# Optimization experiments

Measured on AMD Instinct MI355X. Metric: run time of the kernel, lower is better.

Reference implementation:

```python
import jax, jax.numpy as jnp
import numpy as np

EPS = 1e-5

def _bilinear_sample(xb, ys, xs):
    # xb: [C,H,W]; ys, xs: [H,W] float sample coordinates (zero outside bounds)
    C, H, W = xb.shape
    y0 = jnp.floor(ys); x0 = jnp.floor(xs)
    y1 = y0 + 1.0;      x1 = x0 + 1.0
    wy1 = ys - y0; wy0 = 1.0 - wy1
    wx1 = xs - x0; wx0 = 1.0 - wx1
    def g(yi, xi):
        valid = (yi >= 0) & (yi < H) & (xi >= 0) & (xi < W)
        yc = jnp.clip(yi, 0, H - 1).astype(jnp.int32)
        xc = jnp.clip(xi, 0, W - 1).astype(jnp.int32)
        return xb[:, yc, xc] * valid[None].astype(xb.dtype)  # [C,H,W]
    return (g(y0, x0) * (wy0 * wx0)[None] + g(y0, x1) * (wy0 * wx1)[None]
          + g(y1, x0) * (wy1 * wx0)[None] + g(y1, x1) * (wy1 * wx1)[None])

def _deform_conv2d(x, offset, mask, w, b):
    # x:[B,C,H,W] offset:[B,18,H,W] mask:[B,9,H,W] w:[Co,C,3,3] b:[Co]
    B, C, H, W = x.shape
    Co = w.shape[0]
    ii = jnp.arange(H, dtype=x.dtype)[:, None]
    jj = jnp.arange(W, dtype=x.dtype)[None, :]
    cols = []
    for k in range(9):  # fixed 3x3 kernel positions, row-major (dy=offset[2k], dx=offset[2k+1])
        ky, kx = k // 3 - 1, k % 3 - 1
        ys = ii + ky + offset[:, 2 * k]      # [B,H,W]
        xs = jj + kx + offset[:, 2 * k + 1]
        v = jax.vmap(_bilinear_sample)(x, ys, xs)  # [B,C,H,W]
        cols.append(v * mask[:, k][:, None])
    cols = jnp.stack(cols, axis=1)               # [B,9,C,H,W]
    out = jnp.einsum('bkchw,ock->bohw', cols, w.reshape(Co, C, 9))
    return out + b[None, :, None, None]

def setup_inputs() -> dict:
    key = jax.random.key(0)
    k1, k2, k3, k4 = jax.random.split(key, 4)
    B, Cin, Cout, H, W = 8, 64, 64, 128, 128
    x = jax.random.normal(k1, (B, Cin, H, W), dtype=jnp.float32)
    # offset/mask conv: small weights so learned offsets stay O(1) pixels;
    # bias[18:]=2.0 as in the module's init (masks start near sigmoid(2))
    w_off = jax.random.normal(k2, (27, Cin, 3, 3), dtype=jnp.float32) * 0.01
    b_off = jnp.concatenate([jnp.zeros((18,), jnp.float32), jnp.full((9,), 2.0, jnp.float32)])
    w_dcn = jax.random.normal(k3, (Cout, Cin, 3, 3), dtype=jnp.float32) / np.sqrt(Cin * 9)
    b_dcn = jax.random.normal(k4, (Cout,), dtype=jnp.float32) * 0.01
    return {"x": x, "w_off": w_off, "b_off": b_off, "w_dcn": w_dcn, "b_dcn": b_dcn}

def reference(x, w_off, b_off, w_dcn, b_dcn):
    dn = ('NCHW', 'OIHW', 'NCHW')
    om = jax.lax.conv_general_dilated(x, w_off, (1, 1), 'SAME', dimension_numbers=dn)
    om = om + b_off[None, :, None, None]
    offset = om[:, :18]
    mask = jax.nn.sigmoid(om[:, 18:])
    y = _deform_conv2d(x, offset, mask, w_dcn, b_dcn)
    # InstanceNorm2d (affine=False, biased variance) + ReLU
    mu = jnp.mean(y, axis=(2, 3), keepdims=True)
    var = jnp.var(y, axis=(2, 3), keepdims=True)
    y = (y - mu) * jax.lax.rsqrt(var + EPS)
    return jax.nn.relu(y)
```

## Files before the change

kernel.cpp:

```cpp
#include <hip/hip_runtime.h>
#include <hip/hip_fp16.h>

#define BB   8
#define CIN  64
#define COUT 64
#define HH   128
#define WW   128
#define HWSZ (HH * WW)

typedef _Float16 f16x8 __attribute__((ext_vector_type(8)));
typedef _Float16 h2v   __attribute__((ext_vector_type(2)));
typedef float    f32x4 __attribute__((ext_vector_type(4)));

__device__ __forceinline__ unsigned short f2h_u(float f) {
    __half h = __float2half(f);
    return __half_as_ushort(h);
}
__device__ __forceinline__ float h2f_u(unsigned short u) {
    _Float16 f = *(_Float16*)&u;
    return (float)f;
}
__device__ __forceinline__ unsigned duph(float f) {
    unsigned u = (unsigned)f2h_u(f);
    return u | (u << 16);
}
__device__ __forceinline__ unsigned pk2h(float lo, float hi) {
    return (unsigned)f2h_u(lo) | ((unsigned)f2h_u(hi) << 16);
}
__device__ __forceinline__ h2v dupL(unsigned u) { h2v v = *(h2v*)&u; return (h2v){v[0], v[0]}; }
__device__ __forceinline__ h2v dupH(unsigned u) { h2v v = *(h2v*)&u; return (h2v){v[1], v[1]}; }

__device__ __forceinline__ unsigned comb2h(unsigned a, unsigned b, unsigned c, unsigned d,
                                           h2v W0, h2v W1, h2v W2, h2v W3) {
    h2v A = *(h2v*)&a, B = *(h2v*)&b, C = *(h2v*)&c, D = *(h2v*)&d;
    h2v r = A * W0;
    r += B * W1;
    r += C * W2;
    r += D * W3;
    return *(unsigned*)&r;
}


__global__ __launch_bounds__(256) void k_tr(const float* __restrict__ x,
                                            const float* __restrict__ wd,
                                            const float* __restrict__ wof,
                                            unsigned short* __restrict__ xT,
                                            unsigned short* __restrict__ wdT,
                                            unsigned short* __restrict__ wofT,
                                            float4* __restrict__ sums4)
{
    const int t = threadIdx.x;
    const int id = blockIdx.x;
    if (id >= 512) {
        if (id == 512) sums4[t] = make_float4(0.f, 0.f, 0.f, 0.f);
        int base = (id - 512) * 256 + t;
#pragma unroll
        for (int j = 0; j < 4; ++j) {
            int idx = base + j * 16384;
            if (idx < 36864) {
                int k = idx >> 12, rem = idx & 4095, co = rem >> 6, c = rem & 63;
                wdT[idx] = f2h_u(wd[(co * 64 + c) * 9 + k]);
            } else if (idx < 55296) {
                int jj = idx - 36864;
                int k = jj >> 11, rem = jj & 2047, o = rem >> 6, c = rem & 63;
                wofT[jj] = (o < 27) ? f2h_u(wof[(o * 64 + c) * 9 + k]) : 0;
            }
        }
        return;
    }
    __shared__ unsigned short tile[256 * 66];
    const int b = id & 7;
    const int p0 = (id >> 3) * 256;
#pragma unroll
    for (int i = 0; i < 16; ++i) {
        int c = i * 4 + (t >> 6);
        int pl = (t & 63) * 4;
        float4 v = *(const float4*)(x + (((size_t)b * 64 + c) << 14) + p0 + pl);
        tile[(pl + 0) * 66 + c] = f2h_u(v.x);
        tile[(pl + 1) * 66 + c] = f2h_u(v.y);
        tile[(pl + 2) * 66 + c] = f2h_u(v.z);
        tile[(pl + 3) * 66 + c] = f2h_u(v.w);
    }
    __syncthreads();
#pragma unroll
    for (int i = 0; i < 8; ++i) {
        int idd = i * 256 + t;
        int pt = idd >> 3, ck = idd & 7;
        const unsigned* srcp = (const unsigned*)&tile[pt * 66 + ck * 8];
        uint4 r;
        r.x = srcp[0]; r.y = srcp[1]; r.z = srcp[2]; r.w = srcp[3];
        *(uint4*)(xT + ((size_t)b << 20) + ((size_t)(ck >> 2) << 19)
                     + (size_t)(p0 + pt) * 32 + (ck & 3) * 8) = r;
    }
}

__global__ __launch_bounds__(256, 2) void k_off(
    const unsigned short* __restrict__ xT, const unsigned short* __restrict__ wofT,
    const float* __restrict__ bof, unsigned short* __restrict__ om)
{
    __shared__ unsigned short tile[8 * 521 * 8];
    const int t = threadIdx.x;
    const int lane = t & 63, wv = t >> 6;
    const int q = lane >> 4, l15 = lane & 15;
    const int b = blockIdx.x & 7;
    const int xblk = blockIdx.x >> 3;
    const int h0 = xblk * 2;
    const int r0 = h0 - 1;
    const unsigned short* xb = xT + ((size_t)b << 20);

#pragma unroll
    for (int i = 0; i < 17; ++i) {
        int id = i * 256 + t;
        if (id < 4160) {
            int m = id & 7, lin = id >> 3;
            int row = lin / 130, col = lin % 130;
            int gy = r0 + row, gx = col - 1;
            uint4 v = {0u, 0u, 0u, 0u};
            if (((unsigned)gy < (unsigned)HH) && ((unsigned)gx < (unsigned)WW))
                v = *(const uint4*)(xb + ((size_t)(m >> 2) << 19)
                                       + (size_t)(gy * WW + gx) * 32 + (m & 3) * 8);
            *(uint4*)&tile[(m * 521 + lin) * 8] = v;
        }
    }
    __syncthreads();

    const int hrow = h0 + (wv >> 1);
    const int c0 = (wv & 1) * 64;

    f32x4 acc[2][4];
#pragma unroll
    for (int mt = 0; mt < 2; ++mt)
#pragma unroll
        for (int nt = 0; nt < 4; ++nt) acc[mt][nt] = (f32x4){0.f, 0.f, 0.f, 0.f};

#pragma unroll
    for (int k = 0; k < 9; ++k) {
        const int ky = k / 3 - 1, kx = k % 3 - 1;
        const int trow = (hrow - h0) + ky + 1;
        const unsigned short* wk = wofT + k * 2048;
#pragma unroll
        for (int ks = 0; ks < 2; ++ks) {
            f16x8 af[2], bfr[4];
#pragma unroll
            for (int mt = 0; mt < 2; ++mt)
                af[mt] = *(const f16x8*)(wk + (mt * 16 + l15) * 64 + ks * 32 + q * 8);
#pragma unroll
            for (int nt = 0; nt < 4; ++nt) {
                int tc = c0 + nt * 16 + l15 + kx + 1;
                bfr[nt] = *(const f16x8*)&tile[((ks * 4 + q) * 521 + trow * 130 + tc) * 8];
            }
#pragma unroll
            for (int mt = 0; mt < 2; ++mt)
#pragma unroll
                for (int nt = 0; nt < 4; ++nt)
                    acc[mt][nt] = __builtin_amdgcn_mfma_f32_16x16x32_f16(
                        af[mt], bfr[nt], acc[mt][nt], 0, 0, 0);
        }
    }

    const int p0 = xblk * 256 + wv * 64;
    unsigned short* omb = om + (size_t)b * 27 * HWSZ;
#pragma unroll
    for (int mt = 0; mt < 2; ++mt)
#pragma unroll
        for (int r = 0; r < 4; ++r) {
            int o = mt * 16 + q * 4 + r;
            if (o < 27) {
                float bias = bof[o];
#pragma unroll
                for (int nt = 0; nt < 4; ++nt) {
                    int pp = p0 + nt * 16 + l15;
                    float v = acc[mt][nt][r] + bias;
                    if (o >= 18) v = 1.f / (1.f + __expf(-v));
                    omb[(size_t)o * HWSZ + pp] = f2h_u(v);
                }
            }
        }
}

__global__ __launch_bounds__(256, 2) void k_dcn(
    const unsigned short* __restrict__ xT, const unsigned short* __restrict__ om,
    const unsigned short* __restrict__ wdT, const float* __restrict__ bd,
    float* __restrict__ out, float2* __restrict__ sums)
{
    __shared__ unsigned short tile_sh[6 * 128 * 32];
    __shared__ uint4          meta_sh[4][64];
    __shared__ float          redS[4][64];
    __shared__ float          redQ[4][64];

    const int t = threadIdx.x;
    const int lane = t & 63, wv = t >> 6;
    const int q = lane >> 4, l15 = lane & 15;
    const int b = blockIdx.x & 7;
    const int pblk = (blockIdx.x >> 3) * 256;
    const int p = pblk + t;
    const int h = p >> 7, w = p & 127;
    const int h0 = pblk >> 7;
    const unsigned short* xbS = xT + ((size_t)b << 20);
    const unsigned short* omp = om + (size_t)b * 27 * HWSZ + p;
    const int gch = q * 8;

    f32x4 acc[4][4];
#pragma unroll
    for (int mt = 0; mt < 4; ++mt)
#pragma unroll
        for (int g = 0; g < 4; ++g) acc[mt][g] = (f32x4){0.f, 0.f, 0.f, 0.f};

#define LOADG2(P, g) { \
    unsigned d0_ = M[g].x; \
    unsigned b0_ = (d0_ & 0x000fffffu) + gch; \
    unsigned sx_ = (d0_ >> 19) & 32u;       \
    unsigned sy_ = (d0_ >> 13) & 4096u;     \
    unsigned b1_ = b0_ + sx_; \
    if (__builtin_expect((int)(d0_ >> 31), 0)) { \
        P[0] = *(const uint4*)(xbh + b0_); \
        P[1] = *(const uint4*)(xbh + b1_); \
        P[2] = *(const uint4*)(xbh + b0_ + sy_); \
        P[3] = *(const uint4*)(xbh + b1_ + sy_); \
    } else { \
        P[0] = *(const uint4*)&tile_sh[b0_]; \
        P[1] = *(const uint4*)&tile_sh[b1_]; \
        P[2] = *(const uint4*)&tile_sh[b0_ + sy_]; \
        P[3] = *(const uint4*)&tile_sh[b1_ + sy_]; \
    } }

#define COMB2(DST, P, g) { \
    h2v W0_ = dupL(M[g].y), W2_ = dupH(M[g].y); \
    h2v W1_ = dupL(M[g].z), W3_ = dupH(M[g].z); \
    uint4 R_; \
    R_.x = comb2h(P[0].x, P[1].x, P[2].x, P[3].x, W0_, W1_, W2_, W3_); \
    R_.y = comb2h(P[0].y, P[1].y, P[2].y, P[3].y, W0_, W1_, W2_, W3_); \
    R_.z = comb2h(P[0].z, P[1].z, P[2].z, P[3].z, W0_, W1_, W2_, W3_); \
    R_.w = comb2h(P[0].w, P[1].w, P[2].w, P[3].w, W0_, W1_, W2_, W3_); \
    DST = *(f16x8*)&R_; }

    for (int hf = 0; hf < 2; ++hf) {
        __syncthreads();
        const unsigned short* xbh = xbS + (hf << 19);
#pragma unroll
        for (int i = 0; i < 12; ++i) {
            int idx = i * 256 + t;
            int s = idx >> 9, u = idx & 511;
            int y = h0 - 2 + s;
            y = min(max(y, 0), HH - 1);
            uint4 v = *(const uint4*)(xbh + (size_t)y * (WW * 32) + u * 8);
            *(uint4*)&tile_sh[idx * 8] = v;
        }
        __syncthreads();

        float offy = h2f_u(omp[0]);
        float offx = h2f_u(omp[HWSZ]);
        float mk   = h2f_u(omp[18 * HWSZ]);

        for (int k = 0; k < 9; ++k) {
            float ys = (float)(h + (k / 3) - 1) + offy;
            float xs = (float)(w + (k % 3) - 1) + offx;
            float fy0 = floorf(ys), fx0 = floorf(xs);
            float wy1 = ys - fy0, wx1 = xs - fx0;
            float wy0 = 1.f - wy1, wx0 = 1.f - wx1;
            int y0 = (int)fy0, x0 = (int)fx0;
            int y1 = y0 + 1, x1 = x0 + 1;
            bool vy0 = (y0 >= 0) && (y0 < HH), vy1 = (y1 >= 0) && (y1 < HH);
            bool vx0 = (x0 >= 0) && (x0 < WW), vx1 = (x1 >= 0) && (x1 < WW);
            int y0c = min(max(y0, 0), HH - 1), y1c = min(max(y1, 0), HH - 1);
            int x0c = min(max(x0, 0), WW - 1), x1c = min(max(x1, 0), WW - 1);
            bool ft = (y0c < h0 - 2) || (y1c > h0 + 3);
            unsigned d0;
            if (!ft) d0 = (unsigned)((y0c - h0 + 2) * 4096 + x0c * 32);
            else     d0 = 0x80000000u | (unsigned)((y0c * WW + x0c) * 32);
            if (x1c != x0c) d0 |= 0x01000000u;
            if (y1c != y0c) d0 |= 0x02000000u;
            float w00 = (vy0 && vx0) ? mk * wy0 * wx0 : 0.f;
            float w01 = (vy0 && vx1) ? mk * wy0 * wx1 : 0.f;
            float w10 = (vy1 && vx0) ? mk * wy1 * wx0 : 0.f;
            float w11 = (vy1 && vx1) ? mk * wy1 * wx1 : 0.f;
            meta_sh[wv][lane] = make_uint4(d0, pk2h(w00, w10), pk2h(w01, w11), 0u);
            int kn = (k < 8) ? k + 1 : 8;
            offy = h2f_u(omp[(2 * kn) * HWSZ]);
            offx = h2f_u(omp[(2 * kn + 1) * HWSZ]);
            mk   = h2f_u(omp[(18 + kn) * HWSZ]);
            __builtin_amdgcn_wave_barrier();

            uint4 M[4];
#pragma unroll
            for (int g = 0; g < 4; ++g)
                M[g] = meta_sh[wv][g * 16 + l15];

            const unsigned short* wk = wdT + k * 4096;
            f16x8 af_[4];
#pragma unroll
            for (int mt = 0; mt < 4; ++mt)
                af_[mt] = *(const f16x8*)(wk + (mt * 16 + l15) * 64 + (hf << 5) + q * 8);

            f16x8 bfr[4];
            uint4 pb[3][4];
            LOADG2(pb[0], 0);
            LOADG2(pb[1], 1);
#pragma unroll
            for (int g = 0; g < 4; ++g) {
                if (g + 2 < 4) LOADG2(pb[(g + 2) % 3], g + 2);
                COMB2(bfr[g], pb[g % 3], g);
            }

#pragma unroll
            for (int mt = 0; mt < 4; ++mt)
#pragma unroll
                for (int g = 0; g < 4; ++g)
                    acc[mt][g] = __builtin_amdgcn_mfma_f32_16x16x32_f16(
                        af_[mt], bfr[g], acc[mt][g], 0, 0, 0);
        }
    }
#undef LOADG2
#undef COMB2

    const int p0 = pblk + wv * 64;
    float* outb = out + (size_t)b * COUT * HWSZ;
#pragma unroll
    for (int mt = 0; mt < 4; ++mt)
#pragma unroll
        for (int r = 0; r < 4; ++r) {
            int co = mt * 16 + q * 4 + r;
            float bias = bd[co];
            float s = 0.f, qq = 0.f;
#pragma unroll
            for (int g = 0; g < 4; ++g) {
                float v = acc[mt][g][r] + bias;
                outb[(size_t)co * HWSZ + p0 + g * 16 + l15] = v;
                s += v; qq += v * v;
            }
#pragma unroll
            for (int m = 1; m < 16; m <<= 1) {
                s += __shfl_xor(s, m);
                qq += __shfl_xor(qq, m);
            }
            if (l15 == 0) { redS[wv][co] = s; redQ[wv][co] = qq; }
        }
    __syncthreads();
    if (t < 64) {
        float S = redS[0][t] + redS[1][t] + redS[2][t] + redS[3][t];
        float Q = redQ[0][t] + redQ[1][t] + redQ[2][t] + redQ[3][t];
        atomicAdd(&sums[b * 64 + t].x, S);
        atomicAdd(&sums[b * 64 + t].y, Q);
    }
}

__global__ __launch_bounds__(256) void k_norm(float* __restrict__ out,
                                              const float2* __restrict__ sums)
{
    const int id = blockIdx.x;
    const int b = id & 7;
    const int rest = id >> 3;
    const int co = rest >> 4;
    const int off = rest & 15;
    const int bco = b * 64 + co;
    const int i = (bco << 12) + off * 256 + threadIdx.x;
    float2 sq = sums[bco];
    float mu  = sq.x * (1.f / (float)HWSZ);
    float var = sq.y * (1.f / (float)HWSZ) - mu * mu;
    float rstd = rsqrtf(var + 1e-5f);
    float4* o4 = (float4*)out;
    float4 v = o4[i];
    v.x = fmaxf((v.x - mu) * rstd, 0.f);
    v.y = fmaxf((v.y - mu) * rstd, 0.f);
    v.z = fmaxf((v.z - mu) * rstd, 0.f);
    v.w = fmaxf((v.w - mu) * rstd, 0.f);
    o4[i] = v;
}

extern "C" void kernel_launch(void* const* d_in, const int* in_sizes, int n_in,
                              void* d_out, int out_size, void* d_ws, size_t ws_size,
                              hipStream_t stream) {
    const float* x   = (const float*)d_in[0];
    const float* wof = (const float*)d_in[1];
    const float* bof = (const float*)d_in[2];
    const float* wd  = (const float*)d_in[3];
    const float* bd  = (const float*)d_in[4];
    float* out = (float*)d_out;

    char* ws = (char*)d_ws;
    unsigned short* xT   = (unsigned short*)ws;
    unsigned short* om   = (unsigned short*)(ws + 16777216);
    unsigned short* wdT  = (unsigned short*)(ws + 23855104);
    unsigned short* wofT = (unsigned short*)(ws + 23928832);
    float2*         sums = (float2*)(ws + 23965696);

    k_tr    <<<576, 256, 0, stream>>>(x, wd, wof, xT, wdT, wofT, (float4*)sums);
    k_off   <<<512, 256, 0, stream>>>(xT, wofT, bof, om);
    k_dcn   <<<512, 256, 0, stream>>>(xT, om, wdT, bd, out, sums);
    k_norm  <<<8192, 256, 0, stream>>>(out, (const float2*)sums);
}
```

Before: 149.5 us.

## Store pre-norm DCN output as fp16 and software-pipeline sampling metadata

The deformable conv kernel now writes its pre-normalization output as fp16 to a workspace buffer instead of fp32 to the output. The norm kernel reads that fp16 buffer and writes the final fp32 result, so the intermediate read-modify-write traffic is roughly halved. Separately, the bilinear metadata for the next kernel tap is computed into a double-buffered shared array while the current tap's gathers run, which overlaps address math with memory and MFMA work. The cost is an fp16 rounding of pre-norm values and a larger workspace.

```diff
diff --git a/kernel.cpp b/kernel.cpp
--- a/kernel.cpp
+++ b/kernel.cpp
@@ -19,10 +19,6 @@
 __device__ __forceinline__ float h2f_u(unsigned short u) {
     _Float16 f = *(_Float16*)&u;
     return (float)f;
-}
-__device__ __forceinline__ unsigned duph(float f) {
-    unsigned u = (unsigned)f2h_u(f);
-    return u | (u << 16);
 }
 __device__ __forceinline__ unsigned pk2h(float lo, float hi) {
     return (unsigned)f2h_u(lo) | ((unsigned)f2h_u(hi) << 16);
@@ -181,12 +177,10 @@
 __global__ __launch_bounds__(256, 2) void k_dcn(
     const unsigned short* __restrict__ xT, const unsigned short* __restrict__ om,
     const unsigned short* __restrict__ wdT, const float* __restrict__ bd,
-    float* __restrict__ out, float2* __restrict__ sums)
+    unsigned short* __restrict__ yh, float2* __restrict__ sums)
 {
     __shared__ unsigned short tile_sh[6 * 128 * 32];
-    __shared__ uint4          meta_sh[4][64];
-    __shared__ float          redS[4][64];
-    __shared__ float          redQ[4][64];
+    __shared__ uint4          meta_sh[4][2][64];
 
     const int t = threadIdx.x;
     const int lane = t & 63, wv = t >> 6;
@@ -205,6 +199,34 @@
     for (int mt = 0; mt < 4; ++mt)
 #pragma unroll
         for (int g = 0; g < 4; ++g) acc[mt][g] = (f32x4){0.f, 0.f, 0.f, 0.f};
+
+#define SETUP(kk, buf) { \
+    float ys = (float)(h + ((kk) / 3) - 1) + offy; \
+    float xs = (float)(w + ((kk) % 3) - 1) + offx; \
+    float fy0 = floorf(ys), fx0 = floorf(xs); \
+    float wy1 = ys - fy0, wx1 = xs - fx0; \
+    float wy0 = 1.f - wy1, wx0 = 1.f - wx1; \
+    int y0 = (int)fy0, x0 = (int)fx0; \
+    int y1 = y0 + 1, x1 = x0 + 1; \
+    bool vy0 = (y0 >= 0) && (y0 < HH), vy1 = (y1 >= 0) && (y1 < HH); \
+    bool vx0 = (x0 >= 0) && (x0 < WW), vx1 = (x1 >= 0) && (x1 < WW); \
+    int y0c = min(max(y0, 0), HH - 1), y1c = min(max(y1, 0), HH - 1); \
+    int x0c = min(max(x0, 0), WW - 1), x1c = min(max(x1, 0), WW - 1); \
+    bool ft = (y0c < h0 - 2) || (y1c > h0 + 3); \
+    unsigned d0; \
+    if (!ft) d0 = (unsigned)((y0c - h0 + 2) * 4096 + x0c * 32); \
+    else     d0 = 0x80000000u | (unsigned)((y0c * WW + x0c) * 32); \
+    if (x1c != x0c) d0 |= 0x01000000u; \
+    if (y1c != y0c) d0 |= 0x02000000u; \
+    float w00 = (vy0 && vx0) ? mk * wy0 * wx0 : 0.f; \
+    float w01 = (vy0 && vx1) ? mk * wy0 * wx1 : 0.f; \
+    float w10 = (vy1 && vx0) ? mk * wy1 * wx0 : 0.f; \
+    float w11 = (vy1 && vx1) ? mk * wy1 * wx1 : 0.f; \
+    meta_sh[wv][buf][lane] = make_uint4(d0, pk2h(w00, w10), pk2h(w01, w11), 0u); \
+    int kn = ((kk) < 8) ? (kk) + 1 : 8; \
+    offy = h2f_u(omp[(2 * kn) * HWSZ]); \
+    offx = h2f_u(omp[(2 * kn + 1) * HWSZ]); \
+    mk   = h2f_u(omp[(18 + kn) * HWSZ]); }
 
 #define LOADG2(P, g) { \
     unsigned d0_ = M[g].x; \
@@ -252,40 +274,12 @@
         float offx = h2f_u(omp[HWSZ]);
         float mk   = h2f_u(omp[18 * HWSZ]);
 
+        SETUP(0, 0);
+        uint4 M[4], Mn[4];
+#pragma unroll
+        for (int g = 0; g < 4; ++g) M[g] = meta_sh[wv][0][g * 16 + l15];
+
         for (int k = 0; k < 9; ++k) {
-            float ys = (float)(h + (k / 3) - 1) + offy;
-            float xs = (float)(w + (k % 3) - 1) + offx;
-            float fy0 = floorf(ys), fx0 = floorf(xs);
-            float wy1 = ys - fy0, wx1 = xs - fx0;
-            float wy0 = 1.f - wy1, wx0 = 1.f - wx1;
-            int y0 = (int)fy0, x0 = (int)fx0;
-            int y1 = y0 + 1, x1 = x0 + 1;
-            bool vy0 = (y0 >= 0) && (y0 < HH), vy1 = (y1 >= 0) && (y1 < HH);
-            bool vx0 = (x0 >= 0) && (x0 < WW), vx1 = (x1 >= 0) && (x1 < WW);
-            int y0c = min(max(y0, 0), HH - 1), y1c = min(max(y1, 0), HH - 1);
-            int x0c = min(max(x0, 0), WW - 1), x1c = min(max(x1, 0), WW - 1);
-            bool ft = (y0c < h0 - 2) || (y1c > h0 + 3);
-            unsigned d0;
-            if (!ft) d0 = (unsigned)((y0c - h0 + 2) * 4096 + x0c * 32);
-            else     d0 = 0x80000000u | (unsigned)((y0c * WW + x0c) * 32);
-            if (x1c != x0c) d0 |= 0x01000000u;
-            if (y1c != y0c) d0 |= 0x02000000u;
-            float w00 = (vy0 && vx0) ? mk * wy0 * wx0 : 0.f;
-            float w01 = (vy0 && vx1) ? mk * wy0 * wx1 : 0.f;
-            float w10 = (vy1 && vx0) ? mk * wy1 * wx0 : 0.f;
-            float w11 = (vy1 && vx1) ? mk * wy1 * wx1 : 0.f;
-            meta_sh[wv][lane] = make_uint4(d0, pk2h(w00, w10), pk2h(w01, w11), 0u);
-            int kn = (k < 8) ? k + 1 : 8;
-            offy = h2f_u(omp[(2 * kn) * HWSZ]);
-            offx = h2f_u(omp[(2 * kn + 1) * HWSZ]);
-            mk   = h2f_u(omp[(18 + kn) * HWSZ]);
-            __builtin_amdgcn_wave_barrier();
-
-            uint4 M[4];
-#pragma unroll
-            for (int g = 0; g < 4; ++g)
-                M[g] = meta_sh[wv][g * 16 + l15];
-
             const unsigned short* wk = wdT + k * 4096;
             f16x8 af_[4];
 #pragma unroll
@@ -296,11 +290,17 @@
             uint4 pb[3][4];
             LOADG2(pb[0], 0);
             LOADG2(pb[1], 1);
+            if (k < 8) SETUP(k + 1, (k + 1) & 1);
 #pragma unroll
             for (int g = 0; g < 4; ++g) {
                 if (g + 2 < 4) LOADG2(pb[(g + 2) % 3], g + 2);
                 COMB2(bfr[g], pb[g % 3], g);
             }
+            if (k < 8) {
+#pragma unroll
+                for (int g = 0; g < 4; ++g)
+                    Mn[g] = meta_sh[wv][(k + 1) & 1][g * 16 + l15];
+            }
 
 #pragma unroll
             for (int mt = 0; mt < 4; ++mt)
@@ -308,13 +308,22 @@
                 for (int g = 0; g < 4; ++g)
                     acc[mt][g] = __builtin_amdgcn_mfma_f32_16x16x32_f16(
                         af_[mt], bfr[g], acc[mt][g], 0, 0, 0);
-        }
-    }
+
+            if (k < 8) {
+#pragma unroll
+                for (int g = 0; g < 4; ++g) M[g] = Mn[g];
+            }
+        }
+    }
+#undef SETUP
 #undef LOADG2
 #undef COMB2
 
+    __syncthreads();
+    float* redS = (float*)&meta_sh[0][0][0];
+    float* redQ = redS + 256;
     const int p0 = pblk + wv * 64;
-    float* outb = out + (size_t)b * COUT * HWSZ;
+    unsigned short* yb = yh + (size_t)b * COUT * HWSZ;
 #pragma unroll
     for (int mt = 0; mt < 4; ++mt)
 #pragma unroll
@@ -325,7 +334,7 @@
 #pragma unroll
             for (int g = 0; g < 4; ++g) {
                 float v = acc[mt][g][r] + bias;
-                outb[(size_t)co * HWSZ + p0 + g * 16 + l15] = v;
+                yb[(size_t)co * HWSZ + p0 + g * 16 + l15] = f2h_u(v);
                 s += v; qq += v * v;
             }
 #pragma unroll
@@ -333,38 +342,44 @@
                 s += __shfl_xor(s, m);
                 qq += __shfl_xor(qq, m);
             }
-            if (l15 == 0) { redS[wv][co] = s; redQ[wv][co] = qq; }
+            if (l15 == 0) { redS[wv * 64 + co] = s; redQ[wv * 64 + co] = qq; }
         }
     __syncthreads();
     if (t < 64) {
-        float S = redS[0][t] + redS[1][t] + redS[2][t] + redS[3][t];
-        float Q = redQ[0][t] + redQ[1][t] + redQ[2][t] + redQ[3][t];
+        float S = redS[t] + redS[64 + t] + redS[128 + t] + redS[192 + t];
+        float Q = redQ[t] + redQ[64 + t] + redQ[128 + t] + redQ[192 + t];
         atomicAdd(&sums[b * 64 + t].x, S);
         atomicAdd(&sums[b * 64 + t].y, Q);
     }
 }
 
-__global__ __launch_bounds__(256) void k_norm(float* __restrict__ out,
+__global__ __launch_bounds__(256) void k_norm(const unsigned short* __restrict__ yh,
+                                              float* __restrict__ out,
                                               const float2* __restrict__ sums)
 {
     const int id = blockIdx.x;
     const int b = id & 7;
     const int rest = id >> 3;
-    const int co = rest >> 4;
-    const int off = rest & 15;
+    const int co = rest >> 3;
+    const int off = rest & 7;
     const int bco = b * 64 + co;
-    const int i = (bco << 12) + off * 256 + threadIdx.x;
     float2 sq = sums[bco];
     float mu  = sq.x * (1.f / (float)HWSZ);
     float var = sq.y * (1.f / (float)HWSZ) - mu * mu;
     float rstd = rsqrtf(var + 1e-5f);
-    float4* o4 = (float4*)out;
-    float4 v = o4[i];
-    v.x = fmaxf((v.x - mu) * rstd, 0.f);
-    v.y = fmaxf((v.y - mu) * rstd, 0.f);
-    v.z = fmaxf((v.z - mu) * rstd, 0.f);
-    v.w = fmaxf((v.w - mu) * rstd, 0.f);
-    o4[i] = v;
+    const int base = (bco << 14) + off * 2048 + threadIdx.x * 8;
+    uint4 v8 = *(const uint4*)(yh + base);
+    float4 o0, o1;
+    o0.x = fmaxf((h2f_u((unsigned short)(v8.x & 0xffffu)) - mu) * rstd, 0.f);
+    o0.y = fmaxf((h2f_u((unsigned short)(v8.x >> 16))     - mu) * rstd, 0.f);
+    o0.z = fmaxf((h2f_u((unsigned short)(v8.y & 0xffffu)) - mu) * rstd, 0.f);
+    o0.w = fmaxf((h2f_u((unsigned short)(v8.y >> 16))     - mu) * rstd, 0.f);
+    o1.x = fmaxf((h2f_u((unsigned short)(v8.z & 0xffffu)) - mu) * rstd, 0.f);
+    o1.y = fmaxf((h2f_u((unsigned short)(v8.z >> 16))     - mu) * rstd, 0.f);
+    o1.z = fmaxf((h2f_u((unsigned short)(v8.w & 0xffffu)) - mu) * rstd, 0.f);
+    o1.w = fmaxf((h2f_u((unsigned short)(v8.w >> 16))     - mu) * rstd, 0.f);
+    *(float4*)(out + base)     = o0;
+    *(float4*)(out + base + 4) = o1;
 }
 
 extern "C" void kernel_launch(void* const* d_in, const int* in_sizes, int n_in,
@@ -380,12 +395,13 @@
     char* ws = (char*)d_ws;
     unsigned short* xT   = (unsigned short*)ws;
     unsigned short* om   = (unsigned short*)(ws + 16777216);
-    unsigned short* wdT  = (unsigned short*)(ws + 23855104);
-    unsigned short* wofT = (unsigned short*)(ws + 23928832);
-    float2*         sums = (float2*)(ws + 23965696);
+    unsigned short* yh   = (unsigned short*)(ws + 23855104);
+    unsigned short* wdT  = (unsigned short*)(ws + 40632320);
+    unsigned short* wofT = (unsigned short*)(ws + 40706048);
+    float2*         sums = (float2*)(ws + 40742912);
 
     k_tr    <<<576, 256, 0, stream>>>(x, wd, wof, xT, wdT, wofT, (float4*)sums);
     k_off   <<<512, 256, 0, stream>>>(xT, wofT, bof, om);
-    k_dcn   <<<512, 256, 0, stream>>>(xT, om, wdT, bd, out, sums);
-    k_norm  <<<8192, 256, 0, stream>>>(out, (const float2*)sums);
-}
+    k_dcn   <<<512, 256, 0, stream>>>(xT, om, wdT, bd, yh, sums);
+    k_norm  <<<4096, 256, 0, stream>>>(yh, out, (const float2*)sums);
+}
```

Result: no change. 149.6 us (+0.1%).

## Store pre-norm DCN output as fp16 intermediate and raise occupancy

Applied to the files above, without the earlier changes.

The deform-conv kernel now writes its pre-normalization output to an fp16 workspace buffer instead of fp32 into the final output. The norm kernel reads that half-precision buffer, eight values per thread, and writes fp32. This halves the write traffic of k_dcn and the read traffic of k_norm. The reduction scratch now reuses meta_sh shared memory, which needs an extra barrier, and launch bounds go from 2 to 3 blocks per CU. The cost is fp16 rounding of intermediate activations before normalization, plus register pressure from the tighter bound.

```diff
diff --git a/kernel.cpp b/kernel.cpp
--- a/kernel.cpp
+++ b/kernel.cpp
@@ -19,10 +19,6 @@
 __device__ __forceinline__ float h2f_u(unsigned short u) {
     _Float16 f = *(_Float16*)&u;
     return (float)f;
-}
-__device__ __forceinline__ unsigned duph(float f) {
-    unsigned u = (unsigned)f2h_u(f);
-    return u | (u << 16);
 }
 __device__ __forceinline__ unsigned pk2h(float lo, float hi) {
     return (unsigned)f2h_u(lo) | ((unsigned)f2h_u(hi) << 16);
@@ -178,15 +174,13 @@
         }
 }
 
-__global__ __launch_bounds__(256, 2) void k_dcn(
+__global__ __launch_bounds__(256, 3) void k_dcn(
     const unsigned short* __restrict__ xT, const unsigned short* __restrict__ om,
     const unsigned short* __restrict__ wdT, const float* __restrict__ bd,
-    float* __restrict__ out, float2* __restrict__ sums)
+    unsigned short* __restrict__ yh, float2* __restrict__ sums)
 {
     __shared__ unsigned short tile_sh[6 * 128 * 32];
     __shared__ uint4          meta_sh[4][64];
-    __shared__ float          redS[4][64];
-    __shared__ float          redQ[4][64];
 
     const int t = threadIdx.x;
     const int lane = t & 63, wv = t >> 6;
@@ -313,8 +307,11 @@
 #undef LOADG2
 #undef COMB2
 
+    __syncthreads();
+    float* redS = (float*)&meta_sh[0][0];
+    float* redQ = redS + 256;
     const int p0 = pblk + wv * 64;
-    float* outb = out + (size_t)b * COUT * HWSZ;
+    unsigned short* yb = yh + (size_t)b * COUT * HWSZ;
 #pragma unroll
     for (int mt = 0; mt < 4; ++mt)
 #pragma unroll
@@ -325,7 +322,7 @@
 #pragma unroll
             for (int g = 0; g < 4; ++g) {
                 float v = acc[mt][g][r] + bias;
-                outb[(size_t)co * HWSZ + p0 + g * 16 + l15] = v;
+                yb[(size_t)co * HWSZ + p0 + g * 16 + l15] = f2h_u(v);
                 s += v; qq += v * v;
             }
 #pragma unroll
@@ -333,38 +330,44 @@
                 s += __shfl_xor(s, m);
                 qq += __shfl_xor(qq, m);
             }
-            if (l15 == 0) { redS[wv][co] = s; redQ[wv][co] = qq; }
+            if (l15 == 0) { redS[wv * 64 + co] = s; redQ[wv * 64 + co] = qq; }
         }
     __syncthreads();
     if (t < 64) {
-        float S = redS[0][t] + redS[1][t] + redS[2][t] + redS[3][t];
-        float Q = redQ[0][t] + redQ[1][t] + redQ[2][t] + redQ[3][t];
+        float S = redS[t] + redS[64 + t] + redS[128 + t] + redS[192 + t];
+        float Q = redQ[t] + redQ[64 + t] + redQ[128 + t] + redQ[192 + t];
         atomicAdd(&sums[b * 64 + t].x, S);
         atomicAdd(&sums[b * 64 + t].y, Q);
     }
 }
 
-__global__ __launch_bounds__(256) void k_norm(float* __restrict__ out,
+__global__ __launch_bounds__(256) void k_norm(const unsigned short* __restrict__ yh,
+                                              float* __restrict__ out,
                                               const float2* __restrict__ sums)
 {
     const int id = blockIdx.x;
     const int b = id & 7;
     const int rest = id >> 3;
-    const int co = rest >> 4;
-    const int off = rest & 15;
+    const int co = rest >> 3;
+    const int off = rest & 7;
     const int bco = b * 64 + co;
-    const int i = (bco << 12) + off * 256 + threadIdx.x;
     float2 sq = sums[bco];
     float mu  = sq.x * (1.f / (float)HWSZ);
     float var = sq.y * (1.f / (float)HWSZ) - mu * mu;
     float rstd = rsqrtf(var + 1e-5f);
-    float4* o4 = (float4*)out;
-    float4 v = o4[i];
-    v.x = fmaxf((v.x - mu) * rstd, 0.f);
-    v.y = fmaxf((v.y - mu) * rstd, 0.f);
-    v.z = fmaxf((v.z - mu) * rstd, 0.f);
-    v.w = fmaxf((v.w - mu) * rstd, 0.f);
-    o4[i] = v;
+    const int base = (bco << 14) + off * 2048 + threadIdx.x * 8;
+    uint4 v8 = *(const uint4*)(yh + base);
+    float4 o0, o1;
+    o0.x = fmaxf((h2f_u((unsigned short)(v8.x & 0xffffu)) - mu) * rstd, 0.f);
+    o0.y = fmaxf((h2f_u((unsigned short)(v8.x >> 16))     - mu) * rstd, 0.f);
+    o0.z = fmaxf((h2f_u((unsigned short)(v8.y & 0xffffu)) - mu) * rstd, 0.f);
+    o0.w = fmaxf((h2f_u((unsigned short)(v8.y >> 16))     - mu) * rstd, 0.f);
+    o1.x = fmaxf((h2f_u((unsigned short)(v8.z & 0xffffu)) - mu) * rstd, 0.f);
+    o1.y = fmaxf((h2f_u((unsigned short)(v8.z >> 16))     - mu) * rstd, 0.f);
+    o1.z = fmaxf((h2f_u((unsigned short)(v8.w & 0xffffu)) - mu) * rstd, 0.f);
+    o1.w = fmaxf((h2f_u((unsigned short)(v8.w >> 16))     - mu) * rstd, 0.f);
+    *(float4*)(out + base)     = o0;
+    *(float4*)(out + base + 4) = o1;
 }
 
 extern "C" void kernel_launch(void* const* d_in, const int* in_sizes, int n_in,
@@ -380,12 +383,13 @@
     char* ws = (char*)d_ws;
     unsigned short* xT   = (unsigned short*)ws;
     unsigned short* om   = (unsigned short*)(ws + 16777216);
-    unsigned short* wdT  = (unsigned short*)(ws + 23855104);
-    unsigned short* wofT = (unsigned short*)(ws + 23928832);
-    float2*         sums = (float2*)(ws + 23965696);
+    unsigned short* yh   = (unsigned short*)(ws + 23855104);
+    unsigned short* wdT  = (unsigned short*)(ws + 40632320);
+    unsigned short* wofT = (unsigned short*)(ws + 40706048);
+    float2*         sums = (float2*)(ws + 40742912);
 
     k_tr    <<<576, 256, 0, stream>>>(x, wd, wof, xT, wdT, wofT, (float4*)sums);
     k_off   <<<512, 256, 0, stream>>>(xT, wofT, bof, om);
-    k_dcn   <<<512, 256, 0, stream>>>(xT, om, wdT, bd, out, sums);
-    k_norm  <<<8192, 256, 0, stream>>>(out, (const float2*)sums);
-}
+    k_dcn   <<<512, 256, 0, stream>>>(xT, om, wdT, bd, yh, sums);
+    k_norm  <<<4096, 256, 0, stream>>>(yh, out, (const float2*)sums);
+}
```

Result: slower. 185.3 us (+23.9%).
